# Kernel tuning notes

Hardware: AMD Instinct MI355X
Metric: run time of the kernel (lower is better)

## Reference

```python
import jax, jax.numpy as jnp
import numpy as np

B, CIN, COUT, H, W = 8, 128, 128, 64, 64

# kernel-grid base offsets (dy, dx), row-major k = kh*3 + kw, matching torch base_offset-1
BASE = jnp.array([[-1, -1], [-1, 0], [-1, 1],
                  [0, -1], [0, 0], [0, 1],
                  [1, -1], [1, 0], [1, 1]], dtype=jnp.float32)  # [9,2]
CORNER = jnp.array([1, 0, 1, 0, 0, 0, 1, 0, 1], dtype=jnp.float32)  # mask1 per kernel tap
EDGE = jnp.array([0, 1, 0, 1, 0, 1, 0, 1, 0], dtype=jnp.float32)    # mask2 per kernel tap


def conv3x3(x, w, b=None):
    out = jax.lax.conv_general_dilated(
        x, w, window_strides=(1, 1), padding=((1, 1), (1, 1)),
        dimension_numbers=('NCHW', 'OIHW', 'NCHW'))
    if b is not None:
        out = out + b[None, :, None, None]
    return out


def bilinear_sample(x, py, px):
    Bv, C, Hin, Win = x.shape
    y0 = jnp.floor(py)
    x0 = jnp.floor(px)
    wy = py - y0
    wx = px - x0
    y0i = y0.astype(jnp.int32)
    x0i = x0.astype(jnp.int32)
    xf = x.reshape(Bv, C, Hin * Win)

    def corner(yi, xi):
        valid = ((yi >= 0) & (yi < Hin) & (xi >= 0) & (xi < Win)).astype(x.dtype)
        idx = jnp.clip(yi, 0, Hin - 1) * Win + jnp.clip(xi, 0, Win - 1)  # [B,K,Ho,Wo]
        g = jax.vmap(lambda xb, ib: xb[:, ib])(xf, idx)  # [B,C,K,Ho,Wo]
        return g * valid[:, None]

    v00 = corner(y0i, x0i)
    v01 = corner(y0i, x0i + 1)
    v10 = corner(y0i + 1, x0i)
    v11 = corner(y0i + 1, x0i + 1)
    wy = wy[:, None]
    wx = wx[:, None]
    return (v00 * (1 - wy) * (1 - wx) + v01 * (1 - wy) * wx
            + v10 * wy * (1 - wx) + v11 * wy * wx)


def setup_inputs() -> dict:
    key = jax.random.key(0)
    k1, k2, k3 = jax.random.split(key, 3)
    x = jax.random.normal(k1, (B, CIN, H, W), dtype=jnp.float32)
    # small offset-conv weights keep predicted offsets in a realistic sub-pixel range
    w_off = jax.random.normal(k2, (5, CIN, 3, 3), dtype=jnp.float32) * 0.02
    b_off = jnp.zeros((5,), dtype=jnp.float32)
    w = jax.random.normal(k3, (COUT, CIN, 3, 3), dtype=jnp.float32) * (1.0 / np.sqrt(CIN * 9))
    b = jnp.zeros((COUT,), dtype=jnp.float32)
    return {"x": x, "w_off": w_off, "b_off": b_off, "w": w, "b": b}


def reference(x, w_off, b_off, w, b):
    off = conv3x3(x, w_off, b_off)          # [B,5,H,W]
    scale1 = jax.nn.relu(off[:, 2:3]) + 1.0  # corner scale [B,1,H,W]
    scale2 = jax.nn.relu(off[:, 3:4]) + 1.0  # edge scale   [B,1,H,W]
    shift = off[:, :2]                       # equivariant shift vector [B,2,H,W]

    # per-tap scale; center tap gets 0 but its base offset is (0,0) anyway
    scale_k = CORNER[None, :, None, None] * scale1 + EDGE[None, :, None, None] * scale2  # [B,9,H,W]
    # deform offset = scaled_base - base + shift = base*(scale-1) + shift
    delta = BASE[None, :, :, None, None] * (scale_k - 1.0)[:, :, None] + shift[:, None]  # [B,9,2,H,W]

    hs = jnp.arange(H, dtype=x.dtype)
    ws = jnp.arange(W, dtype=x.dtype)
    # sampling positions: p0 + base_k + offset_k (stride=1, pad=1)
    py = hs[None, None, :, None] + BASE[None, :, 0, None, None] + delta[:, :, 0]  # [B,9,H,W]
    px = ws[None, None, None, :] + BASE[None, :, 1, None, None] + delta[:, :, 1]

    sampled = bilinear_sample(x, py, px)  # [B,CIN,9,H,W]
    out = jnp.einsum('bckhw,ock->bohw', sampled, w.reshape(COUT, CIN, 9))
    return out + b[None, :, None, None]
```

## Files before the change

kernel.cpp:

```cpp
#include <hip/hip_runtime.h>

#define Wd 64
#define Hd 64
#define HWp 4096
#define CIN_ 128
#define COUT_ 128

typedef _Float16 f16;
typedef _Float16 h2    __attribute__((ext_vector_type(2)));
typedef _Float16 f16x8 __attribute__((ext_vector_type(8)));
typedef float f32x4    __attribute__((ext_vector_type(4)));

__device__ inline ushort f2h(float f) {
    f16 h = (f16)f;
    return __builtin_bit_cast(ushort, h);
}
__device__ inline h2 gb(const int4& g, int d) {
    return __builtin_bit_cast(h2, (&g.x)[d]);
}
__device__ inline h2 dup(float f) {
    f16 h = (f16)f;
    h2 r; r[0] = h; r[1] = h;
    return r;
}
struct H8 { h2 r[4]; };

__global__ __launch_bounds__(256) void prep_offsets_kernel(
    const float* __restrict__ x, const float* __restrict__ w,
    const float* __restrict__ w_off, const float* __restrict__ b_off,
    ushort* __restrict__ xt, ushort* __restrict__ w_t2,
    float4* __restrict__ der)
{
    __shared__ char smem[39424];
    int blk = blockIdx.x;
    int t = threadIdx.x;

    if (blk < 576) {
        int i = blk * 256 + t;
        int j    = i & 7;
        int lane = (i >> 3) & 63;
        int ii   = (i >> 9) & 3;
        int wm   = (i >> 11) & 1;
        int s    = i >> 12;
        int o = wm * 64 + ii * 16 + (lane & 15);
        int c = (s & 3) * 32 + (lane >> 4) * 8 + j;
        int k = s >> 2;
        w_t2[i] = f2h(w[o * 1152 + c * 9 + k]);
    } else {
        float* wl    = (float*)smem;
        float* part  = (float*)(smem + 18432);
        ushort* tile = (ushort*)(smem + 22528);
        int blk2 = blk - 576;
        int b = blk2 >> 6;
        int h = blk2 & 63;

        for (int i = t; i < 4608; i += 256) {
            int j = i / 1152;
            int r = i - j * 1152;
            wl[r * 4 + j] = w_off[i];
        }
        __syncthreads();

        int pi = t & 63, cc = t >> 6;
        const float* xb = x + (size_t)(b * CIN_ + cc * 32) * HWp;

        int idx9[9];
        float msk9[9];
        #pragma unroll
        for (int dy = 0; dy < 3; dy++) {
            int hy = h + dy - 1;
            int hyc = min(max(hy, 0), Hd - 1);
            bool vr = (hy >= 0) && (hy < Hd);
            #pragma unroll
            for (int dx = 0; dx < 3; dx++) {
                int wx = pi + dx - 1;
                int wxc = min(max(wx, 0), Wd - 1);
                bool v = vr && (wx >= 0) && (wx < Wd);
                idx9[dy * 3 + dx] = hyc * Wd + wxc;
                msk9[dy * 3 + dx] = v ? 1.0f : 0.0f;
            }
        }

        float o0 = 0.f, o1 = 0.f, o2 = 0.f, o3 = 0.f;
        #pragma unroll 2
        for (int c4 = 0; c4 < 8; c4++) {
            ushort4 hv;
            #pragma unroll
            for (int j = 0; j < 4; j++) {
                int c = c4 * 4 + j;
                const float* xp = xb + c * HWp;
                const float* wc = &wl[(cc * 32 + c) * 36];
                float xv[9];
                #pragma unroll
                for (int tp = 0; tp < 9; tp++) xv[tp] = xp[idx9[tp]] * msk9[tp];
                (&hv.x)[j] = f2h(xv[4]);
                #pragma unroll
                for (int tp = 0; tp < 9; tp++) {
                    float4 wj = *(const float4*)&wc[tp * 4];
                    o0 += xv[tp] * wj.x; o1 += xv[tp] * wj.y;
                    o2 += xv[tp] * wj.z; o3 += xv[tp] * wj.w;
                }
            }
            *(ushort4*)&tile[pi * 132 + cc * 32 + c4 * 4] = hv;
        }
        part[t * 4 + 0] = o0;
        part[t * 4 + 1] = o1;
        part[t * 4 + 2] = o2;
        part[t * 4 + 3] = o3;
        __syncthreads();

        {
            ushort* dst = xt + ((size_t)b * HWp + h * 64) * CIN_;
            #pragma unroll
            for (int k = 0; k < 4; k++) {
                int q = t + k * 256;
                int row = q >> 4, c16 = q & 15;
                int4 v = *(const int4*)&tile[row * 132 + c16 * 8];
                *(int4*)(dst + q * 8) = v;
            }
        }

        if (t < 64) {
            float s0 = b_off[0], s1 = b_off[1], s2 = b_off[2], s3 = b_off[3];
            #pragma unroll
            for (int q = 0; q < 4; q++) {
                s0 += part[(q * 64 + t) * 4 + 0];
                s1 += part[(q * 64 + t) * 4 + 1];
                s2 += part[(q * 64 + t) * 4 + 2];
                s3 += part[(q * 64 + t) * 4 + 3];
            }
            float4 d;
            d.x = s0;
            d.y = s1;
            d.z = fmaxf(s2, 0.f) + 1.f;
            d.w = fmaxf(s3, 0.f) + 1.f;
            der[(size_t)b * HWp + h * Wd + t] = d;
        }
    }
}

__global__ __launch_bounds__(256, 2) void deform_gemm_mfma(
    const ushort* __restrict__ xt, const ushort* __restrict__ w_t2,
    const float* __restrict__ bias, const float4* __restrict__ der,
    float* __restrict__ out)
{
    __shared__ ushort A_lds[2][2][4096];
    __shared__ ushort S_lds[2][2][64 * 40];
    __shared__ int4 MI[9][64];
    __shared__ int4 MW[9][64];

    int t = threadIdx.x;
    int b = blockIdx.x & 7;
    int rp = blockIdx.x >> 3;
    int p0 = rp << 6;
    const char* xtb = (const char*)(xt + (size_t)b * HWp * CIN_);

    int p  = t >> 2;
    int c8 = (t & 3) << 3;
    int c8b = c8 * 2;

    int wv = t >> 6, lane = t & 63;
    int wm = wv & 1, ns = wv >> 1;
    int lm = lane & 15, lq = lane >> 4;

    f32x4 acc[4][2] = {};

    {
        int pg = p0 + p;
        float fh = (float)(pg >> 6), fp = (float)(pg & 63);
        float4 dv = der[(size_t)b * HWp + pg];
        for (int k = (t & 3); k < 9; k += 4) {
            int ky = (k * 11) >> 5;
            int kx = k - ky * 3;
            float by = (float)(ky - 1), bx = (float)(kx - 1);
            bool corner = (ky != 1) && (kx != 1);
            bool edge = (ky != 1) ^ (kx != 1);
            float sk = corner ? dv.z : (edge ? dv.w : 0.0f);
            float py = fh + by * sk + dv.x;
            float px = fp + bx * sk + dv.y;
            float y0f = floorf(py), x0f = floorf(px);
            float wy = py - y0f, wx = px - x0f;
            int y0 = (int)y0f, x0 = (int)x0f;
            int y1 = y0 + 1, x1 = x0 + 1;
            float vy0 = (y0 >= 0 && y0 < Hd) ? 1.f : 0.f;
            float vy1 = (y1 >= 0 && y1 < Hd) ? 1.f : 0.f;
            float vx0 = (x0 >= 0 && x0 < Wd) ? 1.f : 0.f;
            float vx1 = (x1 >= 0 && x1 < Wd) ? 1.f : 0.f;
            int cy0 = min(max(y0, 0), Hd - 1), cy1 = min(max(y1, 0), Hd - 1);
            int cx0 = min(max(x0, 0), Wd - 1), cx1 = min(max(x1, 0), Wd - 1);
            int4 ii;
            ii.x = (cy0 * Wd + cx0) << 8;
            ii.y = (cy0 * Wd + cx1) << 8;
            ii.z = (cy1 * Wd + cx0) << 8;
            ii.w = (cy1 * Wd + cx1) << 8;
            MI[k][p] = ii;
            H8 hw;
            hw.r[0] = dup((1.f - wy) * (1.f - wx) * vy0 * vx0);
            hw.r[1] = dup((1.f - wy) * wx * vy0 * vx1);
            hw.r[2] = dup(wy * (1.f - wx) * vy1 * vx0);
            hw.r[3] = dup(wy * wx * vy1 * vx1);
            MW[k][p] = __builtin_bit_cast(int4, hw);
        }
    }
    __syncthreads();

    int vo0, vo1, vo2, vo3;

    auto stageA = [&](int buf, int st) {
        const ushort* src = w_t2 + (size_t)st * 8192;
        #pragma unroll
        for (int cc = 0; cc < 2; cc++) {
            #pragma unroll
            for (int hrow = 0; hrow < 2; hrow++) {
                const ushort* g = src + cc * 4096 + (wv * 2 + hrow) * 512 + lane * 8;
                ushort* l = &A_lds[buf][cc][(wv * 2 + hrow) * 512];
                __builtin_amdgcn_global_load_lds(
                    (const __attribute__((address_space(1))) unsigned int*)g,
                    (__attribute__((address_space(3))) unsigned int*)l, 16, 0, 0);
            }
        }
    };

    auto issue = [&](int st, int4 (&G)[2][4]) {
        #pragma unroll
        for (int cc = 0; cc < 2; cc++) {
            int q = (2 * st + cc) & 3;
            G[cc][0] = *(const int4*)(xtb + (vo0 + q * 64));
            G[cc][1] = *(const int4*)(xtb + (vo1 + q * 64));
            G[cc][2] = *(const int4*)(xtb + (vo2 + q * 64));
            G[cc][3] = *(const int4*)(xtb + (vo3 + q * 64));
        }
    };
    auto commitS = [&](int buf, const int4 (&G)[2][4], const H8& cw) {
        #pragma unroll
        for (int cc = 0; cc < 2; cc++) {
            H8 tmp;
            #pragma unroll
            for (int d = 0; d < 4; d++) {
                h2 r = gb(G[cc][0], d) * cw.r[0];
                r = gb(G[cc][1], d) * cw.r[1] + r;
                r = gb(G[cc][2], d) * cw.r[2] + r;
                r = gb(G[cc][3], d) * cw.r[3] + r;
                tmp.r[d] = r;
            }
            *(int4*)&S_lds[buf][cc][p * 40 + c8] = __builtin_bit_cast(int4, tmp);
        }
    };
    auto mfmaSec = [&](int cur) {
        #pragma unroll
        for (int cc = 0; cc < 2; cc++) {
            f16x8 af[4], bfr[2];
            #pragma unroll
            for (int i = 0; i < 4; i++)
                af[i] = *(const f16x8*)&A_lds[cur][cc][(wm * 4 + i) * 512 + lane * 8];
            #pragma unroll
            for (int f = 0; f < 2; f++)
                bfr[f] = *(const f16x8*)&S_lds[cur][cc][(ns * 32 + f * 16 + lm) * 40 + lq * 8];
            #pragma unroll
            for (int i = 0; i < 4; i++)
                #pragma unroll
                for (int f = 0; f < 2; f++)
                    acc[i][f] = __builtin_amdgcn_mfma_f32_16x16x32_f16(
                        af[i], bfr[f], acc[i][f], 0, 0, 0);
        }
    };

    int4 GA[2][4], GB[2][4];
    H8 cwA, cwB;
    int4 idxN;

    stageA(0, 0);
    __builtin_amdgcn_sched_barrier(0);
    {
        int4 i0 = MI[0][p];
        vo0 = i0.x + c8b; vo1 = i0.y + c8b; vo2 = i0.z + c8b; vo3 = i0.w + c8b;
    }
    issue(0, GA);
    cwA = __builtin_bit_cast(H8, MW[0][p]);
    commitS(0, GA, cwA);
    issue(1, GB);
    idxN = MI[1][p];
    asm volatile("s_waitcnt vmcnt(8) lgkmcnt(0)" ::: "memory");
    __builtin_amdgcn_s_barrier();
    __builtin_amdgcn_sched_barrier(0);

#define BODY(ST, GC, GI, CWC, CWR, DORD)                                     \
    {                                                                        \
        int cur_ = (ST) & 1, nb_ = cur_ ^ 1;                                 \
        if ((ST) + 1 < 18) stageA(nb_, (ST) + 1);                            \
        __builtin_amdgcn_sched_barrier(0);                                   \
        if ((ST) + 2 < 18) {                                                 \
            if (DORD) {                                                      \
                vo0 = idxN.x + c8b; vo1 = idxN.y + c8b;                      \
                vo2 = idxN.z + c8b; vo3 = idxN.w + c8b;                      \
            }                                                                \
            issue((ST) + 2, GI);                                             \
        }                                                                    \
        if (DORD) {                                                          \
            idxN = MI[min(((ST) >> 1) + 2, 8)][p];                           \
            CWR = __builtin_bit_cast(H8, MW[min(((ST) >> 1) + 1, 8)][p]);    \
        }                                                                    \
        __builtin_amdgcn_s_setprio(1);                                       \
        mfmaSec(cur_);                                                       \
        __builtin_amdgcn_s_setprio(0);                                       \
        if ((ST) + 1 < 18) commitS(nb_, GC, CWC);                            \
        if ((ST) + 2 < 18) {                                                 \
            asm volatile("s_waitcnt vmcnt(8) lgkmcnt(0)" ::: "memory");      \
        } else {                                                             \
            asm volatile("s_waitcnt vmcnt(0) lgkmcnt(0)" ::: "memory");      \
        }                                                                    \
        __builtin_amdgcn_s_barrier();                                        \
        __builtin_amdgcn_sched_barrier(0);                                   \
    }

    for (int su = 0; su < 4; su++) {
        int st = su << 2;
        BODY(st,     GB, GA, cwA, cwB, 1);
        BODY(st + 1, GA, GB, cwB, cwB, 0);
        BODY(st + 2, GB, GA, cwB, cwA, 1);
        BODY(st + 3, GA, GB, cwA, cwA, 0);
    }
    BODY(16, GB, GA, cwA, cwB, 1);
    BODY(17, GA, GB, cwB, cwB, 0);
#undef BODY

    #pragma unroll
    for (int i = 0; i < 4; i++) {
        #pragma unroll
        for (int r = 0; r < 4; r++) {
            int o = wm * 64 + i * 16 + lq * 4 + r;
            float bv = bias[o];
            float* orow = out + (size_t)(b * COUT_ + o) * HWp + p0 + ns * 32 + lm;
            #pragma unroll
            for (int f = 0; f < 2; f++)
                __builtin_nontemporal_store(acc[i][f][r] + bv, &orow[f * 16]);
        }
    }
}

extern "C" void kernel_launch(void* const* d_in, const int* in_sizes, int n_in,
                              void* d_out, int out_size, void* d_ws, size_t ws_size,
                              hipStream_t stream) {
    const float* x     = (const float*)d_in[0];
    const float* w_off = (const float*)d_in[1];
    const float* b_off = (const float*)d_in[2];
    const float* w     = (const float*)d_in[3];
    const float* bias  = (const float*)d_in[4];
    float* out = (float*)d_out;

    char* ws = (char*)d_ws;
    ushort* xt   = (ushort*)ws;
    ushort* w_t2 = (ushort*)(ws + 8388608);
    float4* der  = (float4*)(ws + 8683520);

    prep_offsets_kernel<<<1088, 256, 0, stream>>>(x, w, w_off, b_off,
                                                  xt, w_t2, der);
    deform_gemm_mfma<<<512, 256, 0, stream>>>(xt, w_t2, bias, der, out);
}
```

Baseline: 111.1 us.

## Widen prep blocks to 512 threads, vectorize weight transpose, reorder block mapping

The prep kernel now runs 512-thread blocks. Each offset-conv block splits channels into 8 groups of 16 instead of 4 groups of 32, so each thread handles half as many channels and the partial-sum reduction covers 8 slices. The weight conversion now has each thread produce 8 fp16 values and write them with one 16-byte store, which cuts the block count for that part from 576 to 40. Block-to-(b,h) mapping is also interleaved by batch. The aim is more parallelism per row and fewer narrow stores, at the cost of more shared memory per block and possibly lower occupancy.

```diff
diff --git a/kernel.cpp b/kernel.cpp
--- a/kernel.cpp
+++ b/kernel.cpp
@@ -25,44 +25,49 @@
 }
 struct H8 { h2 r[4]; };
 
-__global__ __launch_bounds__(256) void prep_offsets_kernel(
+__global__ __launch_bounds__(512) void prep_offsets_kernel(
     const float* __restrict__ x, const float* __restrict__ w,
     const float* __restrict__ w_off, const float* __restrict__ b_off,
     ushort* __restrict__ xt, ushort* __restrict__ w_t2,
     float4* __restrict__ der)
 {
-    __shared__ char smem[39424];
+    __shared__ char smem[43520];
     int blk = blockIdx.x;
     int t = threadIdx.x;
 
-    if (blk < 576) {
-        int i = blk * 256 + t;
-        int j    = i & 7;
-        int lane = (i >> 3) & 63;
-        int ii   = (i >> 9) & 3;
-        int wm   = (i >> 11) & 1;
-        int s    = i >> 12;
-        int o = wm * 64 + ii * 16 + (lane & 15);
-        int c = (s & 3) * 32 + (lane >> 4) * 8 + j;
-        int k = s >> 2;
-        w_t2[i] = f2h(w[o * 1152 + c * 9 + k]);
+    if (blk < 40) {
+        int i8 = blk * 512 + t;
+        if (i8 < 18432) {
+            int lane = i8 & 63;
+            int ii   = (i8 >> 6) & 3;
+            int wm   = (i8 >> 8) & 1;
+            int s    = i8 >> 9;
+            int o  = wm * 64 + ii * 16 + (lane & 15);
+            int cb = (s & 3) * 32 + (lane >> 4) * 8;
+            int k  = s >> 2;
+            ushort tmp[8];
+            #pragma unroll
+            for (int j = 0; j < 8; j++)
+                tmp[j] = f2h(w[o * 1152 + (cb + j) * 9 + k]);
+            *(int4*)&w_t2[(size_t)i8 * 8] = *(int4*)tmp;
+        }
     } else {
         float* wl    = (float*)smem;
         float* part  = (float*)(smem + 18432);
-        ushort* tile = (ushort*)(smem + 22528);
-        int blk2 = blk - 576;
-        int b = blk2 >> 6;
-        int h = blk2 & 63;
-
-        for (int i = t; i < 4608; i += 256) {
+        ushort* tile = (ushort*)(smem + 26624);
+        int blk2 = blk - 40;
+        int b = blk2 & 7;
+        int h = blk2 >> 3;
+
+        for (int i = t; i < 4608; i += 512) {
             int j = i / 1152;
             int r = i - j * 1152;
             wl[r * 4 + j] = w_off[i];
         }
         __syncthreads();
 
-        int pi = t & 63, cc = t >> 6;
-        const float* xb = x + (size_t)(b * CIN_ + cc * 32) * HWp;
+        int pi = t & 63, cg = t >> 6;
+        const float* xb = x + (size_t)(b * CIN_ + cg * 16) * HWp;
 
         int idx9[9];
         float msk9[9];
@@ -82,14 +87,14 @@
         }
 
         float o0 = 0.f, o1 = 0.f, o2 = 0.f, o3 = 0.f;
-        #pragma unroll 2
-        for (int c4 = 0; c4 < 8; c4++) {
+        #pragma unroll
+        for (int c4 = 0; c4 < 4; c4++) {
             ushort4 hv;
             #pragma unroll
             for (int j = 0; j < 4; j++) {
                 int c = c4 * 4 + j;
                 const float* xp = xb + c * HWp;
-                const float* wc = &wl[(cc * 32 + c) * 36];
+                const float* wc = &wl[(cg * 16 + c) * 36];
                 float xv[9];
                 #pragma unroll
                 for (int tp = 0; tp < 9; tp++) xv[tp] = xp[idx9[tp]] * msk9[tp];
@@ -101,7 +106,7 @@
                     o2 += xv[tp] * wj.z; o3 += xv[tp] * wj.w;
                 }
             }
-            *(ushort4*)&tile[pi * 132 + cc * 32 + c4 * 4] = hv;
+            *(ushort4*)&tile[pi * 132 + cg * 16 + c4 * 4] = hv;
         }
         part[t * 4 + 0] = o0;
         part[t * 4 + 1] = o1;
@@ -112,8 +117,8 @@
         {
             ushort* dst = xt + ((size_t)b * HWp + h * 64) * CIN_;
             #pragma unroll
-            for (int k = 0; k < 4; k++) {
-                int q = t + k * 256;
+            for (int k = 0; k < 2; k++) {
+                int q = t + k * 512;
                 int row = q >> 4, c16 = q & 15;
                 int4 v = *(const int4*)&tile[row * 132 + c16 * 8];
                 *(int4*)(dst + q * 8) = v;
@@ -123,7 +128,7 @@
         if (t < 64) {
             float s0 = b_off[0], s1 = b_off[1], s2 = b_off[2], s3 = b_off[3];
             #pragma unroll
-            for (int q = 0; q < 4; q++) {
+            for (int q = 0; q < 8; q++) {
                 s0 += part[(q * 64 + t) * 4 + 0];
                 s1 += part[(q * 64 + t) * 4 + 1];
                 s2 += part[(q * 64 + t) * 4 + 2];
@@ -353,7 +358,7 @@
     ushort* w_t2 = (ushort*)(ws + 8388608);
     float4* der  = (float4*)(ws + 8683520);
 
-    prep_offsets_kernel<<<1088, 256, 0, stream>>>(x, w, w_off, b_off,
-                                                  xt, w_t2, der);
+    prep_offsets_kernel<<<552, 512, 0, stream>>>(x, w, w_off, b_off,
+                                                 xt, w_t2, der);
     deform_gemm_mfma<<<512, 256, 0, stream>>>(xt, w_t2, bias, der, out);
 }
```

Result: faster. 108.7 us (-2.1%).
